# Kernel tuning notes

Measured on AMD Instinct MI355X. Metric: run time of the kernel, lower is better.

The kernel has to match this reference:

```python
import jax, jax.numpy as jnp
import numpy as np

B, CH, N = 8, 256, 2048


def setup_inputs() -> dict:
    key = jax.random.key(0)
    kk, kq, kv = jax.random.split(key, 3)
    k = jax.random.normal(kk, (B, CH, N), dtype=jnp.float32)
    q = jax.random.normal(kq, (B, N, CH), dtype=jnp.float32)
    v = jax.random.normal(kv, (B, N, CH), dtype=jnp.float32)
    return {"k": k, "q": q, "v": v}


def reference(k, q, v):
    # 'embedded' mode: attn = softmax(ch^-0.5 * q @ k), dropout p=0 is identity
    ch = k.shape[1]
    scale = ch ** (-0.5)
    attn = jax.nn.softmax(scale * jnp.einsum('bnc,bcm->bnm', q, k), axis=-1)  # [B, N, N]
    attended = jnp.einsum('bnm,bmc->bnc', attn, v)  # [B, N, CH]
    return jnp.transpose(attended, (0, 2, 1))  # [B, CH, N]
```

## Files before the change

### kernel.cpp

```cpp
#include <hip/hip_runtime.h>

namespace {

constexpr int kB = 8;
constexpr int kCH = 256;
constexpr int kN = 2048;
constexpr int NSPLIT = 2;
constexpr int SLICE = kN / NSPLIT;
constexpr int KVC = 64;
constexpr int NWAVE = 4;
constexpr int PS_STRIDE = KVC + 8;

constexpr float SCALE = 0.0625f;
constexpr float LOG2E = 1.4426950408889634f;

typedef _Float16 f16x8 __attribute__((ext_vector_type(8)));
typedef _Float16 f16x4 __attribute__((ext_vector_type(4)));
typedef float f32x4 __attribute__((ext_vector_type(4)));

__device__ __forceinline__ void gload_lds16(const void* g, void* l) {
  __builtin_amdgcn_global_load_lds(
      (const __attribute__((address_space(1))) void*)g,
      (__attribute__((address_space(3))) void*)l, 16, 0, 0);
}

__global__ __launch_bounds__(256) void transpose_cvt2(
    const float* __restrict__ in, _Float16* __restrict__ out, int R, int C) {
  __shared__ _Float16 T[64][72];
  const int b = blockIdx.z;
  const int r0 = blockIdx.y * 64, c0 = blockIdx.x * 64;
  const int t = threadIdx.x;

  const float* ib =
      in + (size_t)b * R * C + (size_t)(r0 + (t >> 2)) * C + c0 + (t & 3) * 4;
#pragma unroll
  for (int q = 0; q < 4; ++q) {
    f32x4 v = *(const f32x4*)(ib + q * 16);
    f16x4 w;
    w[0] = (_Float16)v[0]; w[1] = (_Float16)v[1];
    w[2] = (_Float16)v[2]; w[3] = (_Float16)v[3];
    *(f16x4*)(&T[t >> 2][(t & 3) * 4 + q * 16]) = w;
  }
  __syncthreads();
  const int cl = t >> 2, ch = t & 3;
  f16x8 o0, o1;
#pragma unroll
  for (int j = 0; j < 8; ++j) o0[j] = T[ch * 16 + j][cl];
#pragma unroll
  for (int j = 0; j < 8; ++j) o1[j] = T[ch * 16 + 8 + j][cl];
  _Float16* ob = out + (size_t)b * R * C + (size_t)(c0 + cl) * R + r0 + ch * 16;
  *(f16x8*)(ob) = o0;
  *(f16x8*)(ob + 8) = o1;
}

__global__ __launch_bounds__(256, 2) void attn_part(
    const _Float16* __restrict__ kt, const float* __restrict__ qg,
    const _Float16* __restrict__ vt, _Float16* __restrict__ pacc,
    float* __restrict__ pm, float* __restrict__ pl)
{
  __shared__ alignas(16) char KsB[64 * 512];
  __shared__ alignas(16) char VsB[256 * 128];
  __shared__ alignas(16) _Float16 Ps[NWAVE][16][PS_STRIDE];
  __shared__ float red[NWAVE][16];

  const int tid = threadIdx.x;
  const int wv = tid >> 6;
  const int lane = tid & 63;
  const int s = lane & 15;
  const int qd = lane >> 4;
  const int sw = (s & 7) << 4;
  const int qd16 = qd << 4;

  const int bg = blockIdx.x & 15;
  const int qt = blockIdx.x >> 4;
  const int b = bg >> 1, g = bg & 1;
  const int n0w = qt * 64 + wv * 16;
  const int kvb = g * SLICE;

  const char* ktB = (const char*)(kt + (size_t)b * kN * kCH);
  const char* vtB = (const char*)(vt + (size_t)b * kCH * kN);
  const float* qb = qg + (size_t)b * kN * kCH;

  f16x8 qf[8];
  {
    const float* qrow = qb + (size_t)(n0w + s) * kCH + qd * 8;
#pragma unroll
    for (int ks = 0; ks < 8; ++ks) {
      f32x4 a = *(const f32x4*)(qrow + ks * 32);
      f32x4 c = *(const f32x4*)(qrow + ks * 32 + 4);
      f16x8 h;
      h[0] = (_Float16)a[0]; h[1] = (_Float16)a[1];
      h[2] = (_Float16)a[2]; h[3] = (_Float16)a[3];
      h[4] = (_Float16)c[0]; h[5] = (_Float16)c[1];
      h[6] = (_Float16)c[2]; h[7] = (_Float16)c[3];
      qf[ks] = h;
    }
  }

  f32x4 acc[16];
#pragma unroll
  for (int i = 0; i < 16; ++i) acc[i] = f32x4{0.f, 0.f, 0.f, 0.f};
  float m_r[4] = {-1e30f, -1e30f, -1e30f, -1e30f};
  float l_r[4] = {0.f, 0.f, 0.f, 0.f};

  for (int ck = 0; ck < SLICE / KVC; ++ck) {
    const int kv0 = kvb + ck * KVC;
    __syncthreads();

    {
      const char* kSrc = ktB + (size_t)kv0 * 512;
      const char* vSrc = vtB + (size_t)kv0 * 2;
#pragma unroll
      for (int ii = 0; ii < 8; ++ii) {
        const int j = ii * 4 + wv;
        const int L = j * 1024 + lane * 16;
        {
          const int row = L >> 9, cb = L & 511;
          gload_lds16(kSrc + (size_t)(row << 9) + (cb ^ ((row & 7) << 4)),
                      KsB + j * 1024);
        }
        {
          const int row = L >> 7, cb = L & 127;
          gload_lds16(vSrc + (size_t)row * 4096 + (cb ^ ((row & 7) << 4)),
                      VsB + j * 1024);
        }
      }
    }
    __syncthreads();

    f32x4 sacc[4];
#pragma unroll
    for (int mc = 0; mc < 4; ++mc) sacc[mc] = f32x4{0.f, 0.f, 0.f, 0.f};
#pragma unroll
    for (int mc = 0; mc < 4; ++mc) {
      const char* kr = KsB + (mc * 16 + s) * 512;
#pragma unroll
      for (int ks = 0; ks < 8; ++ks) {
        f16x8 bf = *(const f16x8*)(kr + (((ks << 6) | qd16) ^ sw));
        sacc[mc] = __builtin_amdgcn_mfma_f32_16x16x32_f16(qf[ks], bf, sacc[mc], 0, 0, 0);
      }
    }

    float pmax[4];
#pragma unroll
    for (int r = 0; r < 4; ++r)
      pmax[r] = fmaxf(fmaxf(sacc[0][r], sacc[1][r]), fmaxf(sacc[2][r], sacc[3][r]));
#pragma unroll
    for (int off = 1; off < 16; off <<= 1) {
#pragma unroll
      for (int r = 0; r < 4; ++r)
        pmax[r] = fmaxf(pmax[r], __shfl_xor(pmax[r], off, 64));
    }
    float corr[4], lsum[4];
#pragma unroll
    for (int r = 0; r < 4; ++r) {
      float mn = fmaxf(m_r[r], SCALE * pmax[r]);
      corr[r] = exp2f((m_r[r] - mn) * LOG2E);
      m_r[r] = mn;
      lsum[r] = 0.f;
    }
#pragma unroll
    for (int mc = 0; mc < 4; ++mc) {
#pragma unroll
      for (int r = 0; r < 4; ++r) {
        float pvf = exp2f((SCALE * sacc[mc][r] - m_r[r]) * LOG2E);
        lsum[r] += pvf;
        Ps[wv][qd * 4 + r][mc * 16 + s] = (_Float16)pvf;
      }
    }
#pragma unroll
    for (int off = 1; off < 16; off <<= 1) {
#pragma unroll
      for (int r = 0; r < 4; ++r) lsum[r] += __shfl_xor(lsum[r], off, 64);
    }
#pragma unroll
    for (int r = 0; r < 4; ++r) l_r[r] = l_r[r] * corr[r] + lsum[r];

    if (s == 0) {
#pragma unroll
      for (int r = 0; r < 4; ++r) red[wv][qd * 4 + r] = corr[r];
    }
    asm volatile("s_waitcnt lgkmcnt(0)" ::: "memory");
    const float sc = red[wv][s];
#pragma unroll
    for (int i = 0; i < 16; ++i) acc[i] *= sc;

#pragma unroll
    for (int ms = 0; ms < 2; ++ms) {
      f16x8 pf = *(const f16x8*)(&Ps[wv][s][ms * 32 + qd * 8]);
#pragma unroll
      for (int ct = 0; ct < 16; ++ct) {
        const char* vr = VsB + (ct * 16 + s) * 128;
        f16x8 vf = *(const f16x8*)(vr + (((ms << 6) | qd16) ^ sw));
        acc[ct] = __builtin_amdgcn_mfma_f32_16x16x32_f16(vf, pf, acc[ct], 0, 0, 0);
      }
    }
  }

  _Float16* pb = pacc + (size_t)(b * NSPLIT + g) * kCH * kN;
#pragma unroll
  for (int ct = 0; ct < 16; ++ct) {
#pragma unroll
    for (int r = 0; r < 4; ++r) {
      const int c = ct * 16 + qd * 4 + r;
      pb[(size_t)c * kN + n0w + s] = (_Float16)acc[ct][r];
    }
  }
  if (s == 0) {
#pragma unroll
    for (int r = 0; r < 4; ++r) {
      const int n = n0w + qd * 4 + r;
      pm[((size_t)b * kN + n) * NSPLIT + g] = m_r[r];
      pl[((size_t)b * kN + n) * NSPLIT + g] = l_r[r];
    }
  }
}

__global__ void attn_merge(const _Float16* __restrict__ pacc,
                           const float* __restrict__ pm,
                           const float* __restrict__ pl,
                           float* __restrict__ out) {
  const int b = blockIdx.z;
  const int c = blockIdx.y * 16 + (threadIdx.x >> 4);
  const int nn0 = blockIdx.x * 256 + (threadIdx.x & 15) * 16;

  f16x8 dA[NSPLIT], dB[NSPLIT];
#pragma unroll
  for (int g = 0; g < NSPLIT; ++g) {
    const _Float16* p = pacc + ((size_t)(b * NSPLIT + g) * kCH + c) * kN + nn0;
    dA[g] = *(const f16x8*)(p);
    dB[g] = *(const f16x8*)(p + 8);
  }
  float mv[32], lv[32];
  const float* pmB = pm + ((size_t)b * kN + nn0) * NSPLIT;
  const float* plB = pl + ((size_t)b * kN + nn0) * NSPLIT;
#pragma unroll
  for (int q = 0; q < 8; ++q) {
    *(f32x4*)&mv[q * 4] = *(const f32x4*)(pmB + q * 4);
    *(f32x4*)&lv[q * 4] = *(const f32x4*)(plB + q * 4);
  }
  float res[16];
#pragma unroll
  for (int j = 0; j < 16; ++j) {
    float m0 = mv[2 * j], m1 = mv[2 * j + 1];
    float M = fmaxf(m0, m1);
    float a0 = exp2f((m0 - M) * LOG2E);
    float a1 = exp2f((m1 - M) * LOG2E);
    float L = a0 * lv[2 * j] + a1 * lv[2 * j + 1];
    float v = (j < 8) ? a0 * (float)dA[0][j] + a1 * (float)dA[1][j]
                      : a0 * (float)dB[0][j - 8] + a1 * (float)dB[1][j - 8];
    res[j] = v / L;
  }
  float* o = out + ((size_t)b * kCH + c) * kN + nn0;
#pragma unroll
  for (int j = 0; j < 4; ++j)
    *(f32x4*)(o + j * 4) = f32x4{res[j * 4], res[j * 4 + 1], res[j * 4 + 2], res[j * 4 + 3]};
}

constexpr int QBLK_FB = 64;
constexpr int KVBLK_FB = 64;
constexpr int KS_STRIDE_FB = kCH + 8;
constexpr int VS_STRIDE_FB = KVBLK_FB + 8;

__global__ __launch_bounds__(256, 1) void attn_fwd_fb(
    const float* __restrict__ kg, const float* __restrict__ qg,
    const float* __restrict__ vg, float* __restrict__ og)
{
  __shared__ alignas(16) _Float16 Ks[KVBLK_FB][KS_STRIDE_FB];
  __shared__ alignas(16) _Float16 Vs[kCH][VS_STRIDE_FB];
  __shared__ alignas(16) _Float16 Psf[NWAVE][16][VS_STRIDE_FB];
  __shared__ float red[NWAVE][16];

  const int tid = threadIdx.x;
  const int wv = tid >> 6, lane = tid & 63, s = lane & 15, qd = lane >> 4;
  const int b = blockIdx.x & 7, qt = blockIdx.x >> 3;
  const int n0w = qt * QBLK_FB + wv * 16;
  const float* kb = kg + (size_t)b * kCH * kN;
  const float* qb = qg + (size_t)b * kN * kCH;
  const float* vb = vg + (size_t)b * kN * kCH;
  float* ob = og + (size_t)b * kCH * kN;

  f16x8 qf[8];
  {
    const float* qrow = qb + (size_t)(n0w + s) * kCH + qd * 8;
#pragma unroll
    for (int ks = 0; ks < 8; ++ks) {
      f32x4 a = *(const f32x4*)(qrow + ks * 32);
      f32x4 c = *(const f32x4*)(qrow + ks * 32 + 4);
      f16x8 h;
      h[0] = (_Float16)a[0]; h[1] = (_Float16)a[1];
      h[2] = (_Float16)a[2]; h[3] = (_Float16)a[3];
      h[4] = (_Float16)c[0]; h[5] = (_Float16)c[1];
      h[6] = (_Float16)c[2]; h[7] = (_Float16)c[3];
      qf[ks] = h;
    }
  }
  f32x4 acc[16];
#pragma unroll
  for (int i = 0; i < 16; ++i) acc[i] = f32x4{0.f, 0.f, 0.f, 0.f};
  float m_r[4] = {-1e30f, -1e30f, -1e30f, -1e30f};
  float l_r[4] = {0.f, 0.f, 0.f, 0.f};

  for (int kv0 = 0; kv0 < kN; kv0 += KVBLK_FB) {
    __syncthreads();
    {
      const int m0 = 4 * (tid >> 4), c0b = 4 * (tid & 15);
#pragma unroll
      for (int p = 0; p < 4; ++p) {
        const int c0 = c0b + 64 * p;
        const float* src = kb + (size_t)c0 * kN + kv0 + m0;
        f32x4 r0 = *(const f32x4*)(src);
        f32x4 r1 = *(const f32x4*)(src + kN);
        f32x4 r2 = *(const f32x4*)(src + 2 * kN);
        f32x4 r3 = *(const f32x4*)(src + 3 * kN);
#pragma unroll
        for (int i = 0; i < 4; ++i) {
          f16x4 w;
          w[0] = (_Float16)r0[i]; w[1] = (_Float16)r1[i];
          w[2] = (_Float16)r2[i]; w[3] = (_Float16)r3[i];
          *(f16x4*)(&Ks[m0 + i][c0]) = w;
        }
      }
    }
    {
      const int m0 = 4 * (tid & 15), c0b = 4 * (tid >> 4);
#pragma unroll
      for (int p = 0; p < 4; ++p) {
        const int c0 = c0b + 64 * p;
        const float* src = vb + (size_t)(kv0 + m0) * kCH + c0;
        f32x4 r0 = *(const f32x4*)(src);
        f32x4 r1 = *(const f32x4*)(src + kCH);
        f32x4 r2 = *(const f32x4*)(src + 2 * kCH);
        f32x4 r3 = *(const f32x4*)(src + 3 * kCH);
#pragma unroll
        for (int i = 0; i < 4; ++i) {
          f16x4 w;
          w[0] = (_Float16)r0[i]; w[1] = (_Float16)r1[i];
          w[2] = (_Float16)r2[i]; w[3] = (_Float16)r3[i];
          *(f16x4*)(&Vs[c0 + i][m0]) = w;
        }
      }
    }
    __syncthreads();

    f32x4 sacc[4];
#pragma unroll
    for (int mc = 0; mc < 4; ++mc) sacc[mc] = f32x4{0.f, 0.f, 0.f, 0.f};
#pragma unroll
    for (int mc = 0; mc < 4; ++mc) {
#pragma unroll
      for (int ks = 0; ks < 8; ++ks) {
        f16x8 bf = *(const f16x8*)(&Ks[mc * 16 + s][ks * 32 + qd * 8]);
        sacc[mc] = __builtin_amdgcn_mfma_f32_16x16x32_f16(qf[ks], bf, sacc[mc], 0, 0, 0);
      }
    }
    float pmax[4];
#pragma unroll
    for (int r = 0; r < 4; ++r)
      pmax[r] = fmaxf(fmaxf(sacc[0][r], sacc[1][r]), fmaxf(sacc[2][r], sacc[3][r]));
#pragma unroll
    for (int off = 1; off < 16; off <<= 1) {
#pragma unroll
      for (int r = 0; r < 4; ++r)
        pmax[r] = fmaxf(pmax[r], __shfl_xor(pmax[r], off, 64));
    }
    float corr[4], lsum[4];
#pragma unroll
    for (int r = 0; r < 4; ++r) {
      float mn = fmaxf(m_r[r], SCALE * pmax[r]);
      corr[r] = exp2f((m_r[r] - mn) * LOG2E);
      m_r[r] = mn;
      lsum[r] = 0.f;
    }
#pragma unroll
    for (int mc = 0; mc < 4; ++mc) {
#pragma unroll
      for (int r = 0; r < 4; ++r) {
        float pvf = exp2f((SCALE * sacc[mc][r] - m_r[r]) * LOG2E);
        lsum[r] += pvf;
        Psf[wv][qd * 4 + r][mc * 16 + s] = (_Float16)pvf;
      }
    }
#pragma unroll
    for (int off = 1; off < 16; off <<= 1) {
#pragma unroll
      for (int r = 0; r < 4; ++r) lsum[r] += __shfl_xor(lsum[r], off, 64);
    }
#pragma unroll
    for (int r = 0; r < 4; ++r) l_r[r] = l_r[r] * corr[r] + lsum[r];
    if (s == 0) {
#pragma unroll
      for (int r = 0; r < 4; ++r) red[wv][qd * 4 + r] = corr[r];
    }
    asm volatile("s_waitcnt lgkmcnt(0)" ::: "memory");
    const float sc = red[wv][s];
#pragma unroll
    for (int i = 0; i < 16; ++i) acc[i] *= sc;
#pragma unroll
    for (int ms = 0; ms < 2; ++ms) {
      f16x8 pf = *(const f16x8*)(&Psf[wv][s][ms * 32 + qd * 8]);
#pragma unroll
      for (int ct = 0; ct < 16; ++ct) {
        f16x8 vf = *(const f16x8*)(&Vs[ct * 16 + s][ms * 32 + qd * 8]);
        acc[ct] = __builtin_amdgcn_mfma_f32_16x16x32_f16(vf, pf, acc[ct], 0, 0, 0);
      }
    }
  }
  if (s == 0) {
#pragma unroll
    for (int r = 0; r < 4; ++r) red[wv][qd * 4 + r] = 1.0f / l_r[r];
  }
  asm volatile("s_waitcnt lgkmcnt(0)" ::: "memory");
  const float inv = red[wv][s];
#pragma unroll
  for (int ct = 0; ct < 16; ++ct) {
#pragma unroll
    for (int r = 0; r < 4; ++r) {
      const int c = ct * 16 + qd * 4 + r;
      ob[(size_t)c * kN + n0w + s] = acc[ct][r] * inv;
    }
  }
}

constexpr size_t KT_ELEMS = (size_t)kB * kN * kCH;
constexpr size_t PACC_ELEMS = (size_t)NSPLIT * kB * kCH * kN;
constexpr size_t PM_ELEMS = (size_t)kB * kN * NSPLIT;
constexpr size_t WS_NEED =
    (2 * KT_ELEMS + PACC_ELEMS) * sizeof(_Float16) + 2 * PM_ELEMS * sizeof(float);

}

extern "C" void kernel_launch(void* const* d_in, const int* in_sizes, int n_in,
                              void* d_out, int out_size, void* d_ws, size_t ws_size,
                              hipStream_t stream) {
  (void)in_sizes; (void)n_in; (void)out_size;
  const float* k = (const float*)d_in[0];
  const float* q = (const float*)d_in[1];
  const float* v = (const float*)d_in[2];
  float* out = (float*)d_out;

  if (ws_size < WS_NEED) {
    hipLaunchKernelGGL(attn_fwd_fb, dim3(kB * (kN / QBLK_FB)), dim3(256), 0, stream,
                       k, q, v, out);
    return;
  }

  _Float16* kt = (_Float16*)d_ws;
  _Float16* vt = kt + KT_ELEMS;
  _Float16* pacc = vt + KT_ELEMS;
  float* pm = (float*)(pacc + PACC_ELEMS);
  float* pl = pm + PM_ELEMS;

  hipLaunchKernelGGL(transpose_cvt2, dim3(kN / 64, kCH / 64, kB), dim3(256), 0, stream,
                     k, kt, kCH, kN);
  hipLaunchKernelGGL(transpose_cvt2, dim3(kCH / 64, kN / 64, kB), dim3(256), 0, stream,
                     v, vt, kN, kCH);
  hipLaunchKernelGGL(attn_part, dim3(kB * (kN / 64) * NSPLIT), dim3(256), 0, stream,
                     kt, q, vt, pacc, pm, pl);
  hipLaunchKernelGGL(attn_merge, dim3(kN / 256, kCH / 16, kB), dim3(256), 0, stream,
                     pacc, pm, pl, out);
}
```

Measured before the change: 178.8 us.

## Double-buffer K/V staging, widen attention blocks, defer rescale, fuse transposes

Measured after the change: 174.1 us. -2.6%, faster.

```diff
diff --git a/kernel.cpp b/kernel.cpp
--- a/kernel.cpp
+++ b/kernel.cpp
@@ -8,11 +8,13 @@
 constexpr int NSPLIT = 2;
 constexpr int SLICE = kN / NSPLIT;
 constexpr int KVC = 64;
-constexpr int NWAVE = 4;
+constexpr int NWAVE = 8;
+constexpr int QBLK = 128;
 constexpr int PS_STRIDE = KVC + 8;
 
 constexpr float SCALE = 0.0625f;
 constexpr float LOG2E = 1.4426950408889634f;
+constexpr float DEFER_THR = 4.0f;
 
 typedef _Float16 f16x8 __attribute__((ext_vector_type(8)));
 typedef _Float16 f16x4 __attribute__((ext_vector_type(4)));
@@ -24,11 +26,17 @@
       (__attribute__((address_space(3))) void*)l, 16, 0, 0);
 }
 
-__global__ __launch_bounds__(256) void transpose_cvt2(
-    const float* __restrict__ in, _Float16* __restrict__ out, int R, int C) {
+__global__ __launch_bounds__(256) void transpose_both(
+    const float* __restrict__ kin, const float* __restrict__ vin,
+    _Float16* __restrict__ kt, _Float16* __restrict__ vt) {
   __shared__ _Float16 T[64][72];
-  const int b = blockIdx.z;
-  const int r0 = blockIdx.y * 64, c0 = blockIdx.x * 64;
+  const bool isV = blockIdx.z >= 8;
+  const int b = isV ? blockIdx.z - 8 : blockIdx.z;
+  const int R = isV ? kN : kCH, C = isV ? kCH : kN;
+  const int r0 = (isV ? blockIdx.x : blockIdx.y) * 64;
+  const int c0 = (isV ? blockIdx.y : blockIdx.x) * 64;
+  const float* in = isV ? vin : kin;
+  _Float16* out = isV ? vt : kt;
   const int t = threadIdx.x;
 
   const float* ib =
@@ -53,13 +61,13 @@
   *(f16x8*)(ob + 8) = o1;
 }
 
-__global__ __launch_bounds__(256, 2) void attn_part(
+__global__ __launch_bounds__(512, 1) void attn_part(
     const _Float16* __restrict__ kt, const float* __restrict__ qg,
     const _Float16* __restrict__ vt, _Float16* __restrict__ pacc,
     float* __restrict__ pm, float* __restrict__ pl)
 {
-  __shared__ alignas(16) char KsB[64 * 512];
-  __shared__ alignas(16) char VsB[256 * 128];
+  __shared__ alignas(16) char KsB[2][64 * 512];
+  __shared__ alignas(16) char VsB[2][256 * 128];
   __shared__ alignas(16) _Float16 Ps[NWAVE][16][PS_STRIDE];
   __shared__ float red[NWAVE][16];
 
@@ -74,7 +82,7 @@
   const int bg = blockIdx.x & 15;
   const int qt = blockIdx.x >> 4;
   const int b = bg >> 1, g = bg & 1;
-  const int n0w = qt * 64 + wv * 16;
+  const int n0w = qt * QBLK + wv * 16;
   const int kvb = g * SLICE;
 
   const char* ktB = (const char*)(kt + (size_t)b * kN * kCH);
@@ -103,37 +111,42 @@
   float m_r[4] = {-1e30f, -1e30f, -1e30f, -1e30f};
   float l_r[4] = {0.f, 0.f, 0.f, 0.f};
 
-  for (int ck = 0; ck < SLICE / KVC; ++ck) {
-    const int kv0 = kvb + ck * KVC;
-    __syncthreads();
-
-    {
-      const char* kSrc = ktB + (size_t)kv0 * 512;
-      const char* vSrc = vtB + (size_t)kv0 * 2;
-#pragma unroll
-      for (int ii = 0; ii < 8; ++ii) {
-        const int j = ii * 4 + wv;
-        const int L = j * 1024 + lane * 16;
-        {
-          const int row = L >> 9, cb = L & 511;
-          gload_lds16(kSrc + (size_t)(row << 9) + (cb ^ ((row & 7) << 4)),
-                      KsB + j * 1024);
-        }
-        {
-          const int row = L >> 7, cb = L & 127;
-          gload_lds16(vSrc + (size_t)row * 4096 + (cb ^ ((row & 7) << 4)),
-                      VsB + j * 1024);
-        }
-      }
-    }
-    __syncthreads();
+  auto STAGE = [&](int bf, int kv0) {
+    const char* kSrc = ktB + (size_t)kv0 * 512;
+    const char* vSrc = vtB + (size_t)kv0 * 2;
+    char* kDst = KsB[bf];
+    char* vDst = VsB[bf];
+#pragma unroll
+    for (int ii = 0; ii < 4; ++ii) {
+      const int j = ii * 8 + wv;
+      const int L = j * 1024 + lane * 16;
+      {
+        const int row = L >> 9, cb = L & 511;
+        gload_lds16(kSrc + (size_t)(row << 9) + (cb ^ ((row & 7) << 4)),
+                    kDst + j * 1024);
+      }
+      {
+        const int row = L >> 7, cb = L & 127;
+        gload_lds16(vSrc + (size_t)row * 4096 + (cb ^ ((row & 7) << 4)),
+                    vDst + j * 1024);
+      }
+    }
+  };
+
+  constexpr int NCHUNK = SLICE / KVC;
+  STAGE(0, kvb);
+  __syncthreads();
+
+  for (int ck = 0; ck < NCHUNK; ++ck) {
+    const int cur = ck & 1;
+    if (ck + 1 < NCHUNK) STAGE(cur ^ 1, kvb + (ck + 1) * KVC);
 
     f32x4 sacc[4];
 #pragma unroll
     for (int mc = 0; mc < 4; ++mc) sacc[mc] = f32x4{0.f, 0.f, 0.f, 0.f};
 #pragma unroll
     for (int mc = 0; mc < 4; ++mc) {
-      const char* kr = KsB + (mc * 16 + s) * 512;
+      const char* kr = KsB[cur] + (mc * 16 + s) * 512;
 #pragma unroll
       for (int ks = 0; ks < 8; ++ks) {
         f16x8 bf = *(const f16x8*)(kr + (((ks << 6) | qd16) ^ sw));
@@ -151,14 +164,31 @@
       for (int r = 0; r < 4; ++r)
         pmax[r] = fmaxf(pmax[r], __shfl_xor(pmax[r], off, 64));
     }
-    float corr[4], lsum[4];
-#pragma unroll
-    for (int r = 0; r < 4; ++r) {
-      float mn = fmaxf(m_r[r], SCALE * pmax[r]);
-      corr[r] = exp2f((m_r[r] - mn) * LOG2E);
-      m_r[r] = mn;
-      lsum[r] = 0.f;
-    }
+
+    bool grow = false;
+#pragma unroll
+    for (int r = 0; r < 4; ++r)
+      grow = grow || (SCALE * pmax[r] > m_r[r] + DEFER_THR);
+    if (__any((int)grow)) {
+      float corr[4];
+#pragma unroll
+      for (int r = 0; r < 4; ++r) {
+        float mn = fmaxf(m_r[r], SCALE * pmax[r]);
+        corr[r] = exp2f((m_r[r] - mn) * LOG2E);
+        m_r[r] = mn;
+        l_r[r] *= corr[r];
+      }
+      if (s == 0) {
+#pragma unroll
+        for (int r = 0; r < 4; ++r) red[wv][qd * 4 + r] = corr[r];
+      }
+      asm volatile("s_waitcnt lgkmcnt(0)" ::: "memory");
+      const float sc = red[wv][s];
+#pragma unroll
+      for (int i = 0; i < 16; ++i) acc[i] *= sc;
+    }
+
+    float lsum[4] = {0.f, 0.f, 0.f, 0.f};
 #pragma unroll
     for (int mc = 0; mc < 4; ++mc) {
 #pragma unroll
@@ -174,27 +204,21 @@
       for (int r = 0; r < 4; ++r) lsum[r] += __shfl_xor(lsum[r], off, 64);
     }
 #pragma unroll
-    for (int r = 0; r < 4; ++r) l_r[r] = l_r[r] * corr[r] + lsum[r];
-
-    if (s == 0) {
-#pragma unroll
-      for (int r = 0; r < 4; ++r) red[wv][qd * 4 + r] = corr[r];
-    }
+    for (int r = 0; r < 4; ++r) l_r[r] += lsum[r];
+
     asm volatile("s_waitcnt lgkmcnt(0)" ::: "memory");
-    const float sc = red[wv][s];
-#pragma unroll
-    for (int i = 0; i < 16; ++i) acc[i] *= sc;
 
 #pragma unroll
     for (int ms = 0; ms < 2; ++ms) {
       f16x8 pf = *(const f16x8*)(&Ps[wv][s][ms * 32 + qd * 8]);
 #pragma unroll
       for (int ct = 0; ct < 16; ++ct) {
-        const char* vr = VsB + (ct * 16 + s) * 128;
+        const char* vr = VsB[cur] + (ct * 16 + s) * 128;
         f16x8 vf = *(const f16x8*)(vr + (((ms << 6) | qd16) ^ sw));
         acc[ct] = __builtin_amdgcn_mfma_f32_16x16x32_f16(vf, pf, acc[ct], 0, 0, 0);
       }
     }
+    __syncthreads();
   }
 
   _Float16* pb = pacc + (size_t)(b * NSPLIT + g) * kCH * kN;
@@ -268,8 +292,8 @@
 {
   __shared__ alignas(16) _Float16 Ks[KVBLK_FB][KS_STRIDE_FB];
   __shared__ alignas(16) _Float16 Vs[kCH][VS_STRIDE_FB];
-  __shared__ alignas(16) _Float16 Psf[NWAVE][16][VS_STRIDE_FB];
-  __shared__ float red[NWAVE][16];
+  __shared__ alignas(16) _Float16 Psf[4][16][VS_STRIDE_FB];
+  __shared__ float red[4][16];
 
   const int tid = threadIdx.x;
   const int wv = tid >> 6, lane = tid & 63, s = lane & 15, qd = lane >> 4;
@@ -451,12 +475,10 @@
   float* pm = (float*)(pacc + PACC_ELEMS);
   float* pl = pm + PM_ELEMS;
 
-  hipLaunchKernelGGL(transpose_cvt2, dim3(kN / 64, kCH / 64, kB), dim3(256), 0, stream,
-                     k, kt, kCH, kN);
-  hipLaunchKernelGGL(transpose_cvt2, dim3(kCH / 64, kN / 64, kB), dim3(256), 0, stream,
-                     v, vt, kN, kCH);
-  hipLaunchKernelGGL(attn_part, dim3(kB * (kN / 64) * NSPLIT), dim3(256), 0, stream,
-                     kt, q, vt, pacc, pm, pl);
+  hipLaunchKernelGGL(transpose_both, dim3(kN / 64, kCH / 64, 16), dim3(256), 0,
+                     stream, k, v, kt, vt);
+  hipLaunchKernelGGL(attn_part, dim3(kB * (kN / QBLK) * NSPLIT), dim3(512), 0,
+                     stream, kt, q, vt, pacc, pm, pl);
   hipLaunchKernelGGL(attn_merge, dim3(kN / 256, kCH / 16, kB), dim3(256), 0, stream,
                      pacc, pm, pl, out);
 }
```
